# Kernel optimization log

Measured on AMD Instinct MI355X. Metric: run time of the kernel, lower is better.

Reference implementation:

```python
import jax, jax.numpy as jnp
import numpy as np


def _gcn_conv(x, edge_index, edge_weight, W, b, n_nodes):
    # PyG GCNConv with normalize=True: add self-loops (weight 1), symmetric norm,
    # transform then aggregate: out[col] += norm * (x @ W)[row], plus bias.
    row = jnp.concatenate([edge_index[0], jnp.arange(n_nodes)])
    col = jnp.concatenate([edge_index[1], jnp.arange(n_nodes)])
    w = jnp.concatenate([edge_weight, jnp.ones((n_nodes,), x.dtype)])
    deg = jax.ops.segment_sum(w, col, num_segments=n_nodes)
    dinv = jnp.where(deg > 0, jax.lax.rsqrt(jnp.maximum(deg, 1e-12)), 0.0)
    norm = dinv[row] * w * dinv[col]            # [E+N]
    h = x @ W                                   # [N, out]
    msg = h[row] * norm[:, None]                # [E+N, out]
    out = jax.ops.segment_sum(msg, col, num_segments=n_nodes)
    return out + b


def setup_inputs() -> dict:
    key = jax.random.key(0)
    ks = jax.random.split(key, 6)
    N, E, F_IN, H, C = 50000, 800000, 512, 128, 40
    features = jax.random.normal(ks[0], (N, F_IN), jnp.float32)
    edge_index = jax.random.randint(ks[1], (2, E), 0, N, jnp.int64)
    edge_weight = jax.random.uniform(ks[2], (E,), jnp.float32)
    W1 = jax.random.normal(ks[3], (F_IN, H), jnp.float32) * 0.05
    b1 = jnp.zeros((H,), jnp.float32)
    W2 = jax.random.normal(ks[4], (H, C), jnp.float32) * 0.05
    b2 = jnp.zeros((C,), jnp.float32)
    return {"features": features, "edge_index": edge_index, "edge_weight": edge_weight,
            "W1": W1, "b1": b1, "W2": W2, "b2": b2}


def reference(features, edge_index, edge_weight, W1, b1, W2, b2):
    n_nodes = features.shape[0]
    x = _gcn_conv(features, edge_index, edge_weight, W1, b1, n_nodes)
    x = jax.nn.relu(x)
    # F.dropout(training=self.training): identity in eval mode
    x = _gcn_conv(x, edge_index, edge_weight, W2, b2, n_nodes)
    return jax.nn.log_softmax(x, axis=1)
```

## Files before the change

kernel.cpp:

```cpp
#include <hip/hip_runtime.h>
#include <math.h>

#define FIN  512
#define HDIM 128
#define CDIM 40
#define CPAD 48
#define CAP  64

typedef __attribute__((ext_vector_type(8))) short shortx8;
typedef __attribute__((ext_vector_type(4))) float f32x4;
typedef __attribute__((ext_vector_type(2))) float floatx2;

__device__ inline unsigned short f2bf(float x) {
    unsigned u = __builtin_bit_cast(unsigned, x);
    unsigned r = u + 0x7fffu + ((u >> 16) & 1u);
    return (unsigned short)(r >> 16);
}
__device__ inline float bfu(unsigned short v) { return __builtin_bit_cast(float, (unsigned)v << 16); }
__device__ inline float bflo(unsigned u) { return __builtin_bit_cast(float, u << 16); }
__device__ inline float bfhi(unsigned u) { return __builtin_bit_cast(float, u & 0xffff0000u); }
__device__ inline float wdec(unsigned p) { return __builtin_bit_cast(float, (p & 0x7fffu) << 16); }
__device__ inline unsigned char f2fp8(float x) {
    return (unsigned char)(__builtin_amdgcn_cvt_pk_fp8_f32(x, x, 0, false) & 0xff);
}
__device__ inline floatx2 fp8x2_dec(unsigned short v) {
    return __builtin_amdgcn_cvt_pk_f32_fp8((int)(unsigned)v, false);
}

__global__ void k_fill(const int* __restrict__ row, const int* __restrict__ col,
                       const float* __restrict__ w,
                       unsigned long long* __restrict__ cursor,
                       unsigned* __restrict__ bkt, int E) {
    int e = blockIdx.x * blockDim.x + threadIdx.x;
    if (e >= E) return;
    const int c = col[e];
    const float we = w[e];
    const unsigned long long wfix = (unsigned long long)(we * 4294967296.0f);
    const unsigned long long old = atomicAdd(&cursor[c], (1ULL << 40) | wfix);
    const int p = (int)(old >> 40);
    const unsigned wb = (__builtin_bit_cast(unsigned, we) + 0x8000u) >> 16;
    if (p < CAP) bkt[(size_t)c * CAP + p] = ((unsigned)row[e] << 15) | (wb & 0x7fffu);
}

#define PREPB 280
__global__ void k_prep(const float* __restrict__ W1, const float* __restrict__ W2,
                       unsigned short* __restrict__ W1T, unsigned short* __restrict__ W2T,
                       const unsigned long long* __restrict__ cursor,
                       int* __restrict__ cnt, float* __restrict__ dinv, int n) {
    const int b = blockIdx.x;
    if (b < PREPB) {
        const int i = b * 256 + threadIdx.x;
        if (i < FIN * HDIM) {
            const int k = i >> 7, nn = i & 127;
            W1T[nn * FIN + k] = f2bf(W1[i]);
        } else {
            const int j = i - FIN * HDIM;
            const int nn = j >> 7, k = j & 127;
            W2T[j] = (nn < CDIM) ? f2bf(W2[k * CDIM + nn]) : (unsigned short)0;
        }
    } else {
        const int i = (b - PREPB) * 256 + threadIdx.x;
        if (i < n) {
            const unsigned long long p = cursor[i];
            cnt[i] = min((int)(p >> 40), CAP);
            const float wsum = (float)(p & ((1ULL << 40) - 1)) * 2.3283064365386963e-10f;
            dinv[i] = rsqrtf(1.0f + wsum);
        }
    }
}

#define G1_LDA 72
__global__ __launch_bounds__(256) void k_gemm1(const float* __restrict__ A,
                                               const unsigned short* __restrict__ W1T,
                                               const float* __restrict__ dinv,
                                               unsigned char* __restrict__ h1f8, int M) {
    __shared__ short As[128 * G1_LDA];
    __shared__ short Bs[128 * G1_LDA];
    const int tid  = threadIdx.x;
    const int wave = tid >> 6;
    const int lane = tid & 63;
    const int quad = lane >> 4;
    const int mr   = lane & 15;
    const int m0w  = (wave & 1) * 64;
    const int n0w  = (wave >> 1) * 64;
    const int m0b  = blockIdx.x * 128;

    const int srow = tid >> 1;
    const int spart = tid & 1;

    f32x4 acc[4][4];
#pragma unroll
    for (int i = 0; i < 4; i++)
#pragma unroll
        for (int j = 0; j < 4; j++) acc[i][j] = (f32x4)0.f;

    const int grow = m0b + srow;
    const bool arow_ok = grow < M;
    const float* ap = A + (size_t)grow * FIN + spart * 32;
    const unsigned short* bp = W1T + (size_t)srow * FIN + spart * 32;

    for (int k0 = 0; k0 < FIN; k0 += 64) {
#pragma unroll
        for (int i = 0; i < 4; i++) {
            float4 v0 = make_float4(0.f, 0.f, 0.f, 0.f), v1 = v0;
            if (arow_ok) {
                v0 = *(const float4*)(ap + k0 + i * 8);
                v1 = *(const float4*)(ap + k0 + i * 8 + 4);
            }
            shortx8 pk;
            pk[0] = (short)f2bf(v0.x); pk[1] = (short)f2bf(v0.y);
            pk[2] = (short)f2bf(v0.z); pk[3] = (short)f2bf(v0.w);
            pk[4] = (short)f2bf(v1.x); pk[5] = (short)f2bf(v1.y);
            pk[6] = (short)f2bf(v1.z); pk[7] = (short)f2bf(v1.w);
            *(shortx8*)&As[srow * G1_LDA + spart * 32 + i * 8] = pk;
        }
#pragma unroll
        for (int i = 0; i < 4; i++)
            *(shortx8*)&Bs[srow * G1_LDA + spart * 32 + i * 8] =
                *(const shortx8*)(bp + k0 + i * 8);
        __syncthreads();

#pragma unroll
        for (int kk = 0; kk < 2; kk++) {
            shortx8 af[4], bfr[4];
#pragma unroll
            for (int mt = 0; mt < 4; mt++)
                af[mt] = *(shortx8*)&As[(m0w + mt * 16 + mr) * G1_LDA + kk * 32 + quad * 8];
#pragma unroll
            for (int nt = 0; nt < 4; nt++)
                bfr[nt] = *(shortx8*)&Bs[(n0w + nt * 16 + mr) * G1_LDA + kk * 32 + quad * 8];
#pragma unroll
            for (int mt = 0; mt < 4; mt++)
#pragma unroll
                for (int nt = 0; nt < 4; nt++)
                    acc[mt][nt] = __builtin_amdgcn_mfma_f32_16x16x32_bf16(
                        af[mt], bfr[nt], acc[mt][nt], 0, 0, 0);
        }
        __syncthreads();
    }
#pragma unroll
    for (int mt = 0; mt < 4; mt++)
#pragma unroll
        for (int r = 0; r < 4; r++) {
            const int om = m0b + m0w + mt * 16 + quad * 4 + r;
            if (om < M) {
                const float dv = dinv[om];
#pragma unroll
                for (int nt = 0; nt < 4; nt++)
                    h1f8[(size_t)om * HDIM + n0w + nt * 16 + mr] = f2fp8(dv * acc[mt][nt][r]);
            }
        }
}

__global__ __launch_bounds__(256) void k_gather1(
    const int* __restrict__ cnt_arr, const unsigned* __restrict__ bkt,
    const unsigned char* __restrict__ h1f8,
    const float* __restrict__ dinv, const float* __restrict__ b1,
    unsigned* __restrict__ x1u, int n_nodes) {
    const int node = blockIdx.x * 4 + (threadIdx.x >> 6);
    const int lane = threadIdx.x & 63;
    if (node >= n_nodes) return;
    const int cnt = cnt_arr[node];
    const unsigned* base = bkt + (size_t)node * CAP;
    const int loff = lane * 2;
    float a0 = 0.f, a1 = 0.f, c0 = 0.f, c1 = 0.f;
    int s = 0;
    for (; s + 8 <= cnt; s += 8) {
        const uint4 qa = *(const uint4*)(base + s);
        const uint4 qb = *(const uint4*)(base + s + 4);
        const unsigned short v0 = *(const unsigned short*)(h1f8 + (size_t)(qa.x >> 15) * HDIM + loff);
        const unsigned short v1 = *(const unsigned short*)(h1f8 + (size_t)(qa.y >> 15) * HDIM + loff);
        const unsigned short v2 = *(const unsigned short*)(h1f8 + (size_t)(qa.z >> 15) * HDIM + loff);
        const unsigned short v3 = *(const unsigned short*)(h1f8 + (size_t)(qa.w >> 15) * HDIM + loff);
        const unsigned short v4 = *(const unsigned short*)(h1f8 + (size_t)(qb.x >> 15) * HDIM + loff);
        const unsigned short v5 = *(const unsigned short*)(h1f8 + (size_t)(qb.y >> 15) * HDIM + loff);
        const unsigned short v6 = *(const unsigned short*)(h1f8 + (size_t)(qb.z >> 15) * HDIM + loff);
        const unsigned short v7 = *(const unsigned short*)(h1f8 + (size_t)(qb.w >> 15) * HDIM + loff);
        const floatx2 f0 = fp8x2_dec(v0), f1 = fp8x2_dec(v1), f2 = fp8x2_dec(v2), f3 = fp8x2_dec(v3);
        const floatx2 f4 = fp8x2_dec(v4), f5 = fp8x2_dec(v5), f6 = fp8x2_dec(v6), f7 = fp8x2_dec(v7);
        a0 += wdec(qa.x) * f0.x + wdec(qa.y) * f1.x + wdec(qa.z) * f2.x + wdec(qa.w) * f3.x;
        a1 += wdec(qa.x) * f0.y + wdec(qa.y) * f1.y + wdec(qa.z) * f2.y + wdec(qa.w) * f3.y;
        c0 += wdec(qb.x) * f4.x + wdec(qb.y) * f5.x + wdec(qb.z) * f6.x + wdec(qb.w) * f7.x;
        c1 += wdec(qb.x) * f4.y + wdec(qb.y) * f5.y + wdec(qb.z) * f6.y + wdec(qb.w) * f7.y;
    }
    for (; s + 4 <= cnt; s += 4) {
        const uint4 qa = *(const uint4*)(base + s);
        const unsigned short v0 = *(const unsigned short*)(h1f8 + (size_t)(qa.x >> 15) * HDIM + loff);
        const unsigned short v1 = *(const unsigned short*)(h1f8 + (size_t)(qa.y >> 15) * HDIM + loff);
        const unsigned short v2 = *(const unsigned short*)(h1f8 + (size_t)(qa.z >> 15) * HDIM + loff);
        const unsigned short v3 = *(const unsigned short*)(h1f8 + (size_t)(qa.w >> 15) * HDIM + loff);
        const floatx2 f0 = fp8x2_dec(v0), f1 = fp8x2_dec(v1), f2 = fp8x2_dec(v2), f3 = fp8x2_dec(v3);
        a0 += wdec(qa.x) * f0.x + wdec(qa.y) * f1.x + wdec(qa.z) * f2.x + wdec(qa.w) * f3.x;
        a1 += wdec(qa.x) * f0.y + wdec(qa.y) * f1.y + wdec(qa.z) * f2.y + wdec(qa.w) * f3.y;
    }
    for (; s < cnt; s++) {
        const unsigned p = base[s];
        const unsigned short v = *(const unsigned short*)(h1f8 + (size_t)(p >> 15) * HDIM + loff);
        const floatx2 f = fp8x2_dec(v);
        a0 += wdec(p) * f.x;
        a1 += wdec(p) * f.y;
    }
    a0 += c0; a1 += c1;
    const float dl = dinv[node];
    const unsigned short vs = *(const unsigned short*)(h1f8 + (size_t)node * HDIM + loff);
    const floatx2 fs = fp8x2_dec(vs);
    a0 = fmaxf(dl * (a0 + fs.x) + b1[loff], 0.f);
    a1 = fmaxf(dl * (a1 + fs.y) + b1[loff + 1], 0.f);
    x1u[(size_t)node * 64 + lane] = (unsigned)f2bf(a0) | ((unsigned)f2bf(a1) << 16);
}

#define G2_LDA 136
__global__ __launch_bounds__(256) void k_gemm2(const unsigned short* __restrict__ x1bf,
                                               const unsigned short* __restrict__ W2T,
                                               const float* __restrict__ dinv,
                                               unsigned short* __restrict__ h2a,
                                               unsigned short* __restrict__ h2b, int M) {
    __shared__ short Xs[128 * G2_LDA];
    __shared__ short Ws[CPAD * G2_LDA];
    const int tid  = threadIdx.x;
    const int wave = tid >> 6;
    const int lane = tid & 63;
    const int quad = lane >> 4;
    const int mr   = lane & 15;
    const int m0b  = blockIdx.x * 128;

    {
        const int srow = tid >> 1, spart = tid & 1;
        const int grow = m0b + srow;
        if (grow < M) {
            const unsigned short* xp = x1bf + (size_t)grow * HDIM + spart * 64;
#pragma unroll
            for (int i = 0; i < 8; i++)
                *(shortx8*)&Xs[srow * G2_LDA + spart * 64 + i * 8] = *(const shortx8*)(xp + i * 8);
        } else {
#pragma unroll
            for (int i = 0; i < 8; i++)
                *(shortx8*)&Xs[srow * G2_LDA + spart * 64 + i * 8] = (shortx8)0;
        }
        for (int idx = tid; idx < CPAD * 16; idx += 256) {
            const int r = idx >> 4, j = idx & 15;
            *(shortx8*)&Ws[r * G2_LDA + j * 8] = *(const shortx8*)(W2T + r * HDIM + j * 8);
        }
    }
    __syncthreads();

    f32x4 acc[2][3];
#pragma unroll
    for (int i = 0; i < 2; i++)
#pragma unroll
        for (int j = 0; j < 3; j++) acc[i][j] = (f32x4)0.f;

    const int m0w = wave * 32;
#pragma unroll
    for (int kk = 0; kk < 4; kk++) {
        shortx8 af[2], bfr[3];
#pragma unroll
        for (int mt = 0; mt < 2; mt++)
            af[mt] = *(shortx8*)&Xs[(m0w + mt * 16 + mr) * G2_LDA + kk * 32 + quad * 8];
#pragma unroll
        for (int nt = 0; nt < 3; nt++)
            bfr[nt] = *(shortx8*)&Ws[(nt * 16 + mr) * G2_LDA + kk * 32 + quad * 8];
#pragma unroll
        for (int mt = 0; mt < 2; mt++)
#pragma unroll
            for (int nt = 0; nt < 3; nt++)
                acc[mt][nt] = __builtin_amdgcn_mfma_f32_16x16x32_bf16(
                    af[mt], bfr[nt], acc[mt][nt], 0, 0, 0);
    }
#pragma unroll
    for (int mt = 0; mt < 2; mt++)
#pragma unroll
        for (int r = 0; r < 4; r++) {
            const int om = m0b + m0w + mt * 16 + quad * 4 + r;
            if (om < M) {
                const float dv = dinv[om];
#pragma unroll
                for (int nt = 0; nt < 2; nt++)
                    h2a[(size_t)om * 32 + nt * 16 + mr] = f2bf(dv * acc[mt][nt][r]);
                if (mr < 8)
                    h2b[(size_t)om * 8 + mr] = f2bf(dv * acc[mt][2][r]);
            }
        }
}

__global__ __launch_bounds__(256) void k_gather2(
    const int* __restrict__ cnt_arr, const unsigned* __restrict__ bkt,
    const unsigned short* __restrict__ h2a, const unsigned short* __restrict__ h2b,
    const float* __restrict__ dinv, const float* __restrict__ b2,
    float* __restrict__ out, int n_nodes) {
    const int node = blockIdx.x * 4 + (threadIdx.x >> 6);
    const int lane = threadIdx.x & 63;
    if (node >= n_nodes) return;
    const bool act = lane < CDIM;
    const int cnt = cnt_arr[node];
    const unsigned* base = bkt + (size_t)node * CAP;
    const unsigned short* hb = (lane < 32) ? (h2a + lane) : (h2b + (lane & 31 & 7));
    const int hstride = (lane < 32) ? 32 : 8;
    float acc = 0.f, accb = 0.f;
    int s = 0;
    for (; s + 4 <= cnt; s += 4) {
        const uint4 q = *(const uint4*)(base + s);
        if (act) {
            acc  += wdec(q.x) * bfu(hb[(size_t)(q.x >> 15) * hstride])
                  + wdec(q.y) * bfu(hb[(size_t)(q.y >> 15) * hstride]);
            accb += wdec(q.z) * bfu(hb[(size_t)(q.z >> 15) * hstride])
                  + wdec(q.w) * bfu(hb[(size_t)(q.w >> 15) * hstride]);
        }
    }
    for (; s < cnt; s++) {
        const unsigned p = base[s];
        if (act) acc += wdec(p) * bfu(hb[(size_t)(p >> 15) * hstride]);
    }
    acc += accb;
    if (act) {
        const float dl = dinv[node];
        acc = dl * (acc + bfu(hb[(size_t)node * hstride])) + b2[lane];
    }
    float m = act ? acc : -INFINITY;
#pragma unroll
    for (int off = 32; off; off >>= 1) m = fmaxf(m, __shfl_xor(m, off));
    float se = act ? expf(acc - m) : 0.f;
#pragma unroll
    for (int off = 32; off; off >>= 1) se += __shfl_xor(se, off);
    if (act) out[(size_t)node * CDIM + lane] = acc - m - logf(se);
}

extern "C" void kernel_launch(void* const* d_in, const int* in_sizes, int n_in,
                              void* d_out, int out_size, void* d_ws, size_t ws_size,
                              hipStream_t stream) {
    const float* features = (const float*)d_in[0];
    const int*   eidx     = (const int*)d_in[1];
    const float* ew       = (const float*)d_in[2];
    const float* W1       = (const float*)d_in[3];
    const float* b1       = (const float*)d_in[4];
    const float* W2       = (const float*)d_in[5];
    const float* b2       = (const float*)d_in[6];
    float* out = (float*)d_out;

    const int Nn = in_sizes[0] / FIN;
    const int E  = in_sizes[2];
    const int* row = eidx;
    const int* col = eidx + E;

    char* ws = (char*)d_ws;
    size_t off = 0;
    auto alloc = [&](size_t bytes) { void* p = ws + off; off += (bytes + 255) & ~(size_t)255; return p; };
    unsigned long long* cursor = (unsigned long long*)alloc((size_t)Nn * 8);
    int*      cnt          = (int*)     alloc((size_t)Nn * 4);
    float*    dinv         = (float*)   alloc((size_t)Nn * 4);
    unsigned* bkt          = (unsigned*)alloc((size_t)Nn * CAP * 4);
    unsigned short* W1T    = (unsigned short*)alloc((size_t)FIN * HDIM * 2);
    unsigned short* W2T    = (unsigned short*)alloc((size_t)CPAD * HDIM * 2);
    unsigned char*  h1f8   = (unsigned char*) alloc((size_t)Nn * HDIM);
    unsigned short* x1bf   = (unsigned short*)alloc((size_t)Nn * HDIM * 2);
    unsigned short* h2a    = (unsigned short*)alloc((size_t)Nn * 32 * 2);
    unsigned short* h2b    = (unsigned short*)alloc((size_t)Nn * 8 * 2);

    hipMemsetAsync(cursor, 0, (size_t)Nn * 8, stream);
    k_fill<<<(E + 255) / 256, 256, 0, stream>>>(row, col, ew, cursor, bkt, E);
    k_prep<<<PREPB + (Nn + 255) / 256, 256, 0, stream>>>(W1, W2, W1T, W2T,
                                                         cursor, cnt, dinv, Nn);
    k_gemm1<<<(Nn + 127) / 128, 256, 0, stream>>>(features, W1T, dinv, h1f8, Nn);
    k_gather1<<<(Nn + 3) / 4, 256, 0, stream>>>(cnt, bkt, h1f8, dinv, b1,
                                                (unsigned*)x1bf, Nn);
    k_gemm2<<<(Nn + 127) / 128, 256, 0, stream>>>(x1bf, W2T, dinv, h2a, h2b, Nn);
    k_gather2<<<(Nn + 3) / 4, 256, 0, stream>>>(cnt, bkt, h2a, h2b, dinv, b2, out, Nn);
}
```

Measured before the change: 302.3 us.

## Replace LDS-tiled GEMMs with per-wave register-direct MFMA over 16-row strips

Both GEMM kernels drop shared-memory staging and block-level barriers. Each wave now computes a 16-row strip across all output columns, loading A rows and weight fragments straight from global memory into MFMA operands. This removes LDS traffic and __syncthreads, and gemm1 is streamed from HBM at finer granularity. In exchange, weight tiles are reloaded by every wave through the cache rather than shared within a block, the 16x-tile reuse is lost, and the row bounds checks assume N is a multiple of 16.

```diff
diff --git a/kernel.cpp b/kernel.cpp
--- a/kernel.cpp
+++ b/kernel.cpp
@@ -17,8 +17,6 @@
     return (unsigned short)(r >> 16);
 }
 __device__ inline float bfu(unsigned short v) { return __builtin_bit_cast(float, (unsigned)v << 16); }
-__device__ inline float bflo(unsigned u) { return __builtin_bit_cast(float, u << 16); }
-__device__ inline float bfhi(unsigned u) { return __builtin_bit_cast(float, u & 0xffff0000u); }
 __device__ inline float wdec(unsigned p) { return __builtin_bit_cast(float, (p & 0x7fffu) << 16); }
 __device__ inline unsigned char f2fp8(float x) {
     return (unsigned char)(__builtin_amdgcn_cvt_pk_fp8_f32(x, x, 0, false) & 0xff);
@@ -69,87 +67,49 @@
     }
 }
 
-#define G1_LDA 72
 __global__ __launch_bounds__(256) void k_gemm1(const float* __restrict__ A,
                                                const unsigned short* __restrict__ W1T,
                                                const float* __restrict__ dinv,
                                                unsigned char* __restrict__ h1f8, int M) {
-    __shared__ short As[128 * G1_LDA];
-    __shared__ short Bs[128 * G1_LDA];
-    const int tid  = threadIdx.x;
-    const int wave = tid >> 6;
-    const int lane = tid & 63;
+    const int wid = blockIdx.x * 4 + (threadIdx.x >> 6);
+    const int m0  = wid * 16;
+    if (m0 >= M) return;
+    const int lane = threadIdx.x & 63;
     const int quad = lane >> 4;
     const int mr   = lane & 15;
-    const int m0w  = (wave & 1) * 64;
-    const int n0w  = (wave >> 1) * 64;
-    const int m0b  = blockIdx.x * 128;
-
-    const int srow = tid >> 1;
-    const int spart = tid & 1;
-
-    f32x4 acc[4][4];
-#pragma unroll
-    for (int i = 0; i < 4; i++)
-#pragma unroll
-        for (int j = 0; j < 4; j++) acc[i][j] = (f32x4)0.f;
-
-    const int grow = m0b + srow;
-    const bool arow_ok = grow < M;
-    const float* ap = A + (size_t)grow * FIN + spart * 32;
-    const unsigned short* bp = W1T + (size_t)srow * FIN + spart * 32;
-
-    for (int k0 = 0; k0 < FIN; k0 += 64) {
-#pragma unroll
-        for (int i = 0; i < 4; i++) {
-            float4 v0 = make_float4(0.f, 0.f, 0.f, 0.f), v1 = v0;
-            if (arow_ok) {
-                v0 = *(const float4*)(ap + k0 + i * 8);
-                v1 = *(const float4*)(ap + k0 + i * 8 + 4);
-            }
-            shortx8 pk;
-            pk[0] = (short)f2bf(v0.x); pk[1] = (short)f2bf(v0.y);
-            pk[2] = (short)f2bf(v0.z); pk[3] = (short)f2bf(v0.w);
-            pk[4] = (short)f2bf(v1.x); pk[5] = (short)f2bf(v1.y);
-            pk[6] = (short)f2bf(v1.z); pk[7] = (short)f2bf(v1.w);
-            *(shortx8*)&As[srow * G1_LDA + spart * 32 + i * 8] = pk;
-        }
-#pragma unroll
-        for (int i = 0; i < 4; i++)
-            *(shortx8*)&Bs[srow * G1_LDA + spart * 32 + i * 8] =
-                *(const shortx8*)(bp + k0 + i * 8);
-        __syncthreads();
-
-#pragma unroll
-        for (int kk = 0; kk < 2; kk++) {
-            shortx8 af[4], bfr[4];
-#pragma unroll
-            for (int mt = 0; mt < 4; mt++)
-                af[mt] = *(shortx8*)&As[(m0w + mt * 16 + mr) * G1_LDA + kk * 32 + quad * 8];
-#pragma unroll
-            for (int nt = 0; nt < 4; nt++)
-                bfr[nt] = *(shortx8*)&Bs[(n0w + nt * 16 + mr) * G1_LDA + kk * 32 + quad * 8];
-#pragma unroll
-            for (int mt = 0; mt < 4; mt++)
-#pragma unroll
-                for (int nt = 0; nt < 4; nt++)
-                    acc[mt][nt] = __builtin_amdgcn_mfma_f32_16x16x32_bf16(
-                        af[mt], bfr[nt], acc[mt][nt], 0, 0, 0);
-        }
-        __syncthreads();
-    }
-#pragma unroll
-    for (int mt = 0; mt < 4; mt++)
-#pragma unroll
-        for (int r = 0; r < 4; r++) {
-            const int om = m0b + m0w + mt * 16 + quad * 4 + r;
-            if (om < M) {
-                const float dv = dinv[om];
-#pragma unroll
-                for (int nt = 0; nt < 4; nt++)
-                    h1f8[(size_t)om * HDIM + n0w + nt * 16 + mr] = f2fp8(dv * acc[mt][nt][r]);
-            }
-        }
+
+    f32x4 acc[8];
+#pragma unroll
+    for (int i = 0; i < 8; i++) acc[i] = (f32x4)0.f;
+
+    const float* arow = A + (size_t)(m0 + mr) * FIN + quad * 8;
+    const unsigned short* bbase = W1T + (size_t)mr * FIN + quad * 8;
+
+#pragma unroll 2
+    for (int k0 = 0; k0 < FIN; k0 += 32) {
+        const float4 a0 = *(const float4*)(arow + k0);
+        const float4 a1 = *(const float4*)(arow + k0 + 4);
+        shortx8 af;
+        af[0] = (short)f2bf(a0.x); af[1] = (short)f2bf(a0.y);
+        af[2] = (short)f2bf(a0.z); af[3] = (short)f2bf(a0.w);
+        af[4] = (short)f2bf(a1.x); af[5] = (short)f2bf(a1.y);
+        af[6] = (short)f2bf(a1.z); af[7] = (short)f2bf(a1.w);
+        shortx8 bf[8];
+#pragma unroll
+        for (int nt = 0; nt < 8; nt++)
+            bf[nt] = *(const shortx8*)(bbase + (size_t)nt * 16 * FIN + k0);
+#pragma unroll
+        for (int nt = 0; nt < 8; nt++)
+            acc[nt] = __builtin_amdgcn_mfma_f32_16x16x32_bf16(af, bf[nt], acc[nt], 0, 0, 0);
+    }
+#pragma unroll
+    for (int r = 0; r < 4; r++) {
+        const int om = m0 + quad * 4 + r;
+        const float dv = dinv[om];
+#pragma unroll
+        for (int nt = 0; nt < 8; nt++)
+            h1f8[(size_t)om * HDIM + nt * 16 + mr] = f2fp8(dv * acc[nt][r]);
+    }
 }
 
 __global__ __launch_bounds__(256) void k_gather1(
@@ -209,78 +169,44 @@
     x1u[(size_t)node * 64 + lane] = (unsigned)f2bf(a0) | ((unsigned)f2bf(a1) << 16);
 }
 
-#define G2_LDA 136
 __global__ __launch_bounds__(256) void k_gemm2(const unsigned short* __restrict__ x1bf,
                                                const unsigned short* __restrict__ W2T,
                                                const float* __restrict__ dinv,
                                                unsigned short* __restrict__ h2a,
                                                unsigned short* __restrict__ h2b, int M) {
-    __shared__ short Xs[128 * G2_LDA];
-    __shared__ short Ws[CPAD * G2_LDA];
-    const int tid  = threadIdx.x;
-    const int wave = tid >> 6;
-    const int lane = tid & 63;
+    const int wid = blockIdx.x * 4 + (threadIdx.x >> 6);
+    const int m0  = wid * 16;
+    if (m0 >= M) return;
+    const int lane = threadIdx.x & 63;
     const int quad = lane >> 4;
     const int mr   = lane & 15;
-    const int m0b  = blockIdx.x * 128;
-
-    {
-        const int srow = tid >> 1, spart = tid & 1;
-        const int grow = m0b + srow;
-        if (grow < M) {
-            const unsigned short* xp = x1bf + (size_t)grow * HDIM + spart * 64;
-#pragma unroll
-            for (int i = 0; i < 8; i++)
-                *(shortx8*)&Xs[srow * G2_LDA + spart * 64 + i * 8] = *(const shortx8*)(xp + i * 8);
-        } else {
-#pragma unroll
-            for (int i = 0; i < 8; i++)
-                *(shortx8*)&Xs[srow * G2_LDA + spart * 64 + i * 8] = (shortx8)0;
-        }
-        for (int idx = tid; idx < CPAD * 16; idx += 256) {
-            const int r = idx >> 4, j = idx & 15;
-            *(shortx8*)&Ws[r * G2_LDA + j * 8] = *(const shortx8*)(W2T + r * HDIM + j * 8);
-        }
-    }
-    __syncthreads();
-
-    f32x4 acc[2][3];
-#pragma unroll
-    for (int i = 0; i < 2; i++)
-#pragma unroll
-        for (int j = 0; j < 3; j++) acc[i][j] = (f32x4)0.f;
-
-    const int m0w = wave * 32;
-#pragma unroll
-    for (int kk = 0; kk < 4; kk++) {
-        shortx8 af[2], bfr[3];
-#pragma unroll
-        for (int mt = 0; mt < 2; mt++)
-            af[mt] = *(shortx8*)&Xs[(m0w + mt * 16 + mr) * G2_LDA + kk * 32 + quad * 8];
-#pragma unroll
-        for (int nt = 0; nt < 3; nt++)
-            bfr[nt] = *(shortx8*)&Ws[(nt * 16 + mr) * G2_LDA + kk * 32 + quad * 8];
-#pragma unroll
-        for (int mt = 0; mt < 2; mt++)
-#pragma unroll
-            for (int nt = 0; nt < 3; nt++)
-                acc[mt][nt] = __builtin_amdgcn_mfma_f32_16x16x32_bf16(
-                    af[mt], bfr[nt], acc[mt][nt], 0, 0, 0);
-    }
-#pragma unroll
-    for (int mt = 0; mt < 2; mt++)
-#pragma unroll
-        for (int r = 0; r < 4; r++) {
-            const int om = m0b + m0w + mt * 16 + quad * 4 + r;
-            if (om < M) {
-                const float dv = dinv[om];
-#pragma unroll
-                for (int nt = 0; nt < 2; nt++)
-                    h2a[(size_t)om * 32 + nt * 16 + mr] = f2bf(dv * acc[mt][nt][r]);
-                if (mr < 8)
-                    h2b[(size_t)om * 8 + mr] = f2bf(dv * acc[mt][2][r]);
-            }
-        }
+
+    f32x4 acc[3];
+#pragma unroll
+    for (int i = 0; i < 3; i++) acc[i] = (f32x4)0.f;
+
+    const unsigned short* xrow  = x1bf + (size_t)(m0 + mr) * HDIM + quad * 8;
+    const unsigned short* bbase = W2T + (size_t)mr * HDIM + quad * 8;
+
+#pragma unroll
+    for (int k0 = 0; k0 < HDIM; k0 += 32) {
+        const shortx8 af = *(const shortx8*)(xrow + k0);
+#pragma unroll
+        for (int nt = 0; nt < 3; nt++) {
+            const shortx8 bf = *(const shortx8*)(bbase + (size_t)nt * 16 * HDIM + k0);
+            acc[nt] = __builtin_amdgcn_mfma_f32_16x16x32_bf16(af, bf, acc[nt], 0, 0, 0);
+        }
+    }
+#pragma unroll
+    for (int r = 0; r < 4; r++) {
+        const int om = m0 + quad * 4 + r;
+        const float dv = dinv[om];
+#pragma unroll
+        for (int nt = 0; nt < 2; nt++)
+            h2a[(size_t)om * 32 + nt * 16 + mr] = f2bf(dv * acc[nt][r]);
+        if (mr < 8)
+            h2b[(size_t)om * 8 + mr] = f2bf(dv * acc[2][r]);
+    }
 }
 
 __global__ __launch_bounds__(256) void k_gather2(
@@ -294,7 +220,7 @@
     const bool act = lane < CDIM;
     const int cnt = cnt_arr[node];
     const unsigned* base = bkt + (size_t)node * CAP;
-    const unsigned short* hb = (lane < 32) ? (h2a + lane) : (h2b + (lane & 31 & 7));
+    const unsigned short* hb = (lane < 32) ? (h2a + lane) : (h2b + (lane & 7));
     const int hstride = (lane < 32) ? 32 : 8;
     float acc = 0.f, accb = 0.f;
     int s = 0;
@@ -360,9 +286,10 @@
     k_fill<<<(E + 255) / 256, 256, 0, stream>>>(row, col, ew, cursor, bkt, E);
     k_prep<<<PREPB + (Nn + 255) / 256, 256, 0, stream>>>(W1, W2, W1T, W2T,
                                                          cursor, cnt, dinv, Nn);
-    k_gemm1<<<(Nn + 127) / 128, 256, 0, stream>>>(features, W1T, dinv, h1f8, Nn);
+    const int nwave1 = (Nn + 15) / 16;
+    k_gemm1<<<(nwave1 + 3) / 4, 256, 0, stream>>>(features, W1T, dinv, h1f8, Nn);
     k_gather1<<<(Nn + 3) / 4, 256, 0, stream>>>(cnt, bkt, h1f8, dinv, b1,
                                                 (unsigned*)x1bf, Nn);
-    k_gemm2<<<(Nn + 127) / 128, 256, 0, stream>>>(x1bf, W2T, dinv, h2a, h2b, Nn);
+    k_gemm2<<<(nwave1 + 3) / 4, 256, 0, stream>>>(x1bf, W2T, dinv, h2a, h2b, Nn);
     k_gather2<<<(Nn + 3) / 4, 256, 0, stream>>>(cnt, bkt, h2a, h2b, dinv, b2, out, Nn);
 }
```

Result: slower. 343.7 us (+13.7%).
